# Optimization experiments

Hardware: AMD Instinct MI355X
Metric: run time of the kernel (lower is better)

## Reference

```python
import jax, jax.numpy as jnp
import numpy as np

B, N, D = 4, 256, 256
NEG = -1e9


def setup_inputs() -> dict:
    key = jax.random.key(0)
    k = jax.random.split(key, 5)
    scale1 = 1.0 / np.sqrt(4 * D)
    scale2 = 1.0 / np.sqrt(D)
    return {
        "shared": jax.random.normal(k[0], (B, N, D), dtype=jnp.float32),
        "W1": jax.random.uniform(k[1], (4 * D, D), jnp.float32, -scale1, scale1),
        "b1": jax.random.uniform(k[2], (D,), jnp.float32, -scale1, scale1),
        "W2": jax.random.uniform(k[3], (D, 1), jnp.float32, -scale2, scale2),
        "b2": jax.random.uniform(k[4], (1,), jnp.float32, -scale2, scale2),
    }


def reference(shared, W1, b1, W2, b2):
    # Linear on concat([src, tgt, |src-tgt|, src*tgt]) == sum of per-block matmuls.
    Wa, Wb, Wc, Wd = W1[:D], W1[D:2 * D], W1[2 * D:3 * D], W1[3 * D:]
    src_t = jnp.einsum('bid,dh->bih', shared, Wa)        # [B,N,D]
    tgt_t = jnp.einsum('bjd,dh->bjh', shared, Wb)        # [B,N,D]
    diff = jnp.abs(shared[:, :, None, :] - shared[:, None, :, :])  # [B,N,N,D]
    prod = shared[:, :, None, :] * shared[:, None, :, :]           # [B,N,N,D]
    h = (src_t[:, :, None, :] + tgt_t[:, None, :, :]
         + jnp.einsum('bijd,dh->bijh', diff, Wc)
         + jnp.einsum('bijd,dh->bijh', prod, Wd) + b1)   # [B,N,N,D]
    h = jax.nn.silu(h)
    scores = jnp.einsum('bijh,h->bij', h, W2[:, 0]) + b2[0]  # [B,N,N]
    eye = jnp.eye(N, dtype=bool)[None]
    scores = jnp.where(eye, NEG, scores)
    return jax.nn.softmax(scores, axis=-1)
```

## Files before the change

### kernel.cpp

```cpp
#include <hip/hip_runtime.h>

#define BB 4
#define NN 256
#define DD 256
#define HH 256
#define NEGV -1.0e9f

typedef _Float16 half8 __attribute__((ext_vector_type(8)));
typedef __fp16   fp16x2 __attribute__((ext_vector_type(2)));
typedef float floatx4 __attribute__((ext_vector_type(4)));

__global__ __launch_bounds__(1024) void prep(const float* __restrict__ X,
                                             const float* __restrict__ W1,
                                             float* __restrict__ S,
                                             float* __restrict__ T,
                                             _Float16* __restrict__ Wst) {
  const int g = blockIdx.x;
  const int t = threadIdx.x;

  __shared__ float xr[4][256];
  __shared__ float part[2][4][4][256];

  if (t < 256) {
    const float wcv = W1[(size_t)(2 * DD + g) * HH + t];
    const float wdv = W1[(size_t)(3 * DD + g) * HH + t];
    const int ks = g >> 4;
    const int dd = g & 15;
    const int q  = dd >> 2;
    const int e  = (dd & 3) * 2;
    const int hgrp = t >> 4;
    const int ccw  = t & 15;
    _Float16* p = Wst + ((size_t)((ks * 16 + hgrp) * 4 + q) * 16 + ccw) * 8 + e;
    p[0] = (_Float16)wcv;
    p[1] = (_Float16)wdv;
  }

  const int row0 = g * 4;
  xr[t >> 8][t & 255] = X[(size_t)row0 * DD + t];
  __syncthreads();

  const int w    = t >> 6;
  const int lane = t & 63;
  const int r    = w >> 2;
  const int kq   = w & 3;
  const int h0   = lane * 4;
  const float* __restrict__ xrow = xr[r];
  const int dbase = kq * 64;

  float sa0 = 0.f, sa1 = 0.f, sa2 = 0.f, sa3 = 0.f;
  float sb0 = 0.f, sb1 = 0.f, sb2 = 0.f, sb3 = 0.f;
#pragma unroll 4
  for (int dd = 0; dd < 64; ++dd) {
    const int d = dbase + dd;
    const float4 wa = *(const float4*)&W1[(size_t)d * HH + h0];
    const float4 wb = *(const float4*)&W1[(size_t)(DD + d) * HH + h0];
    const float x = xrow[d];
    sa0 = fmaf(x, wa.x, sa0); sa1 = fmaf(x, wa.y, sa1);
    sa2 = fmaf(x, wa.z, sa2); sa3 = fmaf(x, wa.w, sa3);
    sb0 = fmaf(x, wb.x, sb0); sb1 = fmaf(x, wb.y, sb1);
    sb2 = fmaf(x, wb.z, sb2); sb3 = fmaf(x, wb.w, sb3);
  }
  *(float4*)&part[0][r][kq][h0] = make_float4(sa0, sa1, sa2, sa3);
  *(float4*)&part[1][r][kq][h0] = make_float4(sb0, sb1, sb2, sb3);
  __syncthreads();

  const int rr = t >> 8, hh = t & 255;
  S[(size_t)(row0 + rr) * HH + hh] =
      (part[0][rr][0][hh] + part[0][rr][1][hh]) +
      (part[0][rr][2][hh] + part[0][rr][3][hh]);
  T[(size_t)(row0 + rr) * HH + hh] =
      (part[1][rr][0][hh] + part[1][rr][1][hh]) +
      (part[1][rr][2][hh] + part[1][rr][3][hh]);
}

__device__ __forceinline__ half8 make_afrag(const float4 xi, const float4 xj) {
  fp16x2 p0 = __builtin_amdgcn_cvt_pkrtz(__builtin_fabsf(xi.x - xj.x), xi.x * xj.x);
  fp16x2 p1 = __builtin_amdgcn_cvt_pkrtz(__builtin_fabsf(xi.y - xj.y), xi.y * xj.y);
  fp16x2 p2 = __builtin_amdgcn_cvt_pkrtz(__builtin_fabsf(xi.z - xj.z), xi.z * xj.z);
  fp16x2 p3 = __builtin_amdgcn_cvt_pkrtz(__builtin_fabsf(xi.w - xj.w), xi.w * xj.w);
  uint4 u;
  u.x = __builtin_bit_cast(unsigned int, p0);
  u.y = __builtin_bit_cast(unsigned int, p1);
  u.z = __builtin_bit_cast(unsigned int, p2);
  u.w = __builtin_bit_cast(unsigned int, p3);
  return __builtin_bit_cast(half8, u);
}

#define MFMA16(af, bf, acc) acc = __builtin_amdgcn_mfma_f32_16x16x32_f16(af, bf, acc, 0, 0, 0)

template <int CTRL>
__device__ __forceinline__ float dpp_add(float v) {
  const int s = __builtin_amdgcn_update_dpp(0, __builtin_bit_cast(int, v),
                                            CTRL, 0xF, 0xF, true);
  return v + __builtin_bit_cast(float, s);
}

__global__ __launch_bounds__(512, 4) void score_mfma(
    const float* __restrict__ X,  const float* __restrict__ b1,
    const float* __restrict__ W2, const float* __restrict__ b2,
    const float* __restrict__ S,  const float* __restrict__ T,
    const _Float16* __restrict__ Wst, float* __restrict__ Sc) {

  const int beta = blockIdx.x;
  const int b    = blockIdx.y;
  int i, qt;
  if (beta < 64)       { qt = 0; i = beta; }
  else if (beta < 192) { qt = 1; i = beta - 64; }
  else if (beta < 384) { qt = 2; i = beta - 192; }
  else                 { qt = 3; i = beta - 384; }
  const int bi    = b * NN + i;
  const int jbase = qt * 64;
  const int isUp  = qt > (i >> 6);

  const int t     = threadIdx.x;
  const int lane  = t & 63;
  const int hg    = t >> 6;
  const int q     = lane >> 4;
  const int cc    = lane & 15;

  __shared__ __align__(16) float    xi_s[DD];
  __shared__ __align__(16) _Float16 Af[32768];
  __shared__ float pre_s[HH];
  __shared__ float pre2_s[HH];
  __shared__ float w2_s[HH];
  __shared__ float sc_s[8][64];

  if (t < 256) {
    xi_s[t]  = X[(size_t)bi * DD + t];
    pre_s[t] = S[(size_t)bi * HH + t] + b1[t];
  } else {
    const int u = t - 256;
    pre2_s[u] = T[(size_t)bi * HH + u] + b1[u];
    w2_s[u]   = W2[u];
  }

  const float* __restrict__ Tb = T + (size_t)b * NN * HH;
  const float* __restrict__ Sb = S + (size_t)b * NN * HH;

  const int jloc = t & 63;
  const int jg   = jloc >> 4;
  const int ccw  = jloc & 15;
  const float* __restrict__ xjrow = X + (size_t)(b * NN + jbase + jloc) * DD;

  const char* __restrict__ bsrc = (const char*)Wst + hg * 2048 + (size_t)lane * 16;

  half8 Bf0[4], Bf1[4];
#pragma unroll
  for (int u = 0; u < 4; ++u) {
    Bf0[u] = *(const half8*)(bsrc + (size_t)u * 16384);
    Bf1[u] = *(const half8*)(bsrc + (size_t)u * 16384 + 1024);
  }

  __syncthreads();

  {
    const int sgrp = t >> 6;
#pragma unroll
    for (int idx = 0; idx < 8; ++idx) {
      const int ksqg = sgrp * 8 + idx;
      const int d0   = ksqg * 4;
      const int kg   = ksqg >> 2;
      const int qw   = ksqg & 3;
      const float4 xi4 = *(const float4*)&xi_s[d0];
      const float4 xj4 = *(const float4*)(xjrow + d0);
      *(half8*)&Af[kg * 2048 + (jg * 4 + qw) * 128 + ccw * 8] = make_afrag(xi4, xj4);
    }
  }
  __syncthreads();

  floatx4 acc0[4], acc1[4];
#pragma unroll
  for (int u = 0; u < 4; ++u) { acc0[u] = (floatx4)0.f; acc1[u] = (floatx4)0.f; }

  const _Float16* ap0 = &Af[lane * 8];
  half8 An0 = *(const half8*)(ap0);
  half8 An1 = *(const half8*)(ap0 + 512);
  half8 An2 = *(const half8*)(ap0 + 1024);
  half8 An3 = *(const half8*)(ap0 + 1536);

#pragma unroll
  for (int kg = 0; kg < 16; ++kg) {
    const int s = kg & 3;
    const half8 Bc0 = Bf0[s], Bc1 = Bf1[s];
    const half8 Ac0 = An0, Ac1 = An1, Ac2 = An2, Ac3 = An3;
    if (kg < 12) {
      const char* bk = bsrc + (size_t)(kg + 4) * 16384;
      Bf0[s] = *(const half8*)(bk);
      Bf1[s] = *(const half8*)(bk + 1024);
    }
    if (kg < 15) {
      const _Float16* ap = &Af[(kg + 1) * 2048 + lane * 8];
      An0 = *(const half8*)(ap);
      An1 = *(const half8*)(ap + 512);
      An2 = *(const half8*)(ap + 1024);
      An3 = *(const half8*)(ap + 1536);
    }
    MFMA16(Ac0, Bc0, acc0[0]); MFMA16(Ac0, Bc1, acc1[0]);
    MFMA16(Ac1, Bc0, acc0[1]); MFMA16(Ac1, Bc1, acc1[1]);
    MFMA16(Ac2, Bc0, acc0[2]); MFMA16(Ac2, Bc1, acc1[2]);
    MFMA16(Ac3, Bc0, acc0[3]); MFMA16(Ac3, Bc1, acc1[3]);
  }

  const int h0   = hg * 32 + cc;
  const int h1   = h0 + 16;
  const int jrow = jbase + q * 4;

#define EPILOGUE(VROW, PRE) {                                                   \
    float tv0[16], tv1[16];                                                     \
    _Pragma("unroll")                                                           \
    for (int u = 0; u < 16; ++u) {                                              \
      const size_t j = (size_t)(jrow + (u >> 2) * 16 + (u & 3)) * HH;           \
      tv0[u] = VROW[j + h0];                                                    \
      tv1[u] = VROW[j + h1];                                                    \
    }                                                                           \
    const float w20 = w2_s[h0], pv0 = PRE[h0];                                  \
    const float w21 = w2_s[h1], pv1 = PRE[h1];                                  \
    float p[16];                                                                \
    _Pragma("unroll")                                                           \
    for (int u = 0; u < 16; ++u) {                                              \
      const float hv0 = acc0[u >> 2][u & 3] + pv0 + tv0[u];                     \
      const float sv0 = hv0 * __builtin_amdgcn_rcpf(1.f + __expf(-hv0));        \
      p[u] = sv0 * w20;                                                         \
      const float hv1 = acc1[u >> 2][u & 3] + pv1 + tv1[u];                     \
      const float sv1 = hv1 * __builtin_amdgcn_rcpf(1.f + __expf(-hv1));        \
      p[u] = fmaf(sv1, w21, p[u]);                                              \
    }                                                                           \
    _Pragma("unroll")                                                           \
    for (int u = 0; u < 16; ++u) {                                              \
      float v = p[u];                                                           \
      v = dpp_add<0xB1>(v);                       \
      v = dpp_add<0x4E>(v);                       \
      v = dpp_add<0x141>(v);              \
      v = dpp_add<0x140>(v);                   \
      if (cc == 0) sc_s[hg][(u >> 2) * 16 + q * 4 + (u & 3)] = v;               \
    } }

  EPILOGUE(Tb, pre_s)
  __syncthreads();

  if (t < 64) {
    float s = sc_s[0][t] + sc_s[1][t] + sc_s[2][t] + sc_s[3][t]
            + sc_s[4][t] + sc_s[5][t] + sc_s[6][t] + sc_s[7][t] + b2[0];
    const int jg2 = jbase + t;
    if (jg2 == i) s = NEGV;
    Sc[(size_t)bi * NN + jg2] = s;
  }

  if (isUp) {
    __syncthreads();
    EPILOGUE(Sb, pre2_s)
    __syncthreads();
    if (t < 64) {
      const float s = sc_s[0][t] + sc_s[1][t] + sc_s[2][t] + sc_s[3][t]
                    + sc_s[4][t] + sc_s[5][t] + sc_s[6][t] + sc_s[7][t] + b2[0];
      Sc[(size_t)(b * NN + jbase + t) * NN + i] = s;
    }
  }
#undef EPILOGUE
}

__global__ __launch_bounds__(256) void softmax_kernel(const float* __restrict__ Sc,
                                                      float* __restrict__ out) {
  const int w    = threadIdx.x >> 6;
  const int lane = threadIdx.x & 63;
  const int bi   = blockIdx.x * 4 + w;
  const float4 v = *(const float4*)&Sc[(size_t)bi * NN + lane * 4];
  float m = fmaxf(fmaxf(v.x, v.y), fmaxf(v.z, v.w));
  m = fmaxf(m, __shfl_xor(m, 1));  m = fmaxf(m, __shfl_xor(m, 2));
  m = fmaxf(m, __shfl_xor(m, 4));  m = fmaxf(m, __shfl_xor(m, 8));
  m = fmaxf(m, __shfl_xor(m, 16)); m = fmaxf(m, __shfl_xor(m, 32));
  const float e0 = __expf(v.x - m), e1 = __expf(v.y - m);
  const float e2 = __expf(v.z - m), e3 = __expf(v.w - m);
  float sum = (e0 + e1) + (e2 + e3);
  sum += __shfl_xor(sum, 1);  sum += __shfl_xor(sum, 2);
  sum += __shfl_xor(sum, 4);  sum += __shfl_xor(sum, 8);
  sum += __shfl_xor(sum, 16); sum += __shfl_xor(sum, 32);
  const float r = 1.f / sum;
  float4 o; o.x = e0 * r; o.y = e1 * r; o.z = e2 * r; o.w = e3 * r;
  *(float4*)&out[(size_t)bi * NN + lane * 4] = o;
}

extern "C" void kernel_launch(void* const* d_in, const int* in_sizes, int n_in,
                              void* d_out, int out_size, void* d_ws, size_t ws_size,
                              hipStream_t stream) {
  const float* X  = (const float*)d_in[0];
  const float* W1 = (const float*)d_in[1];
  const float* b1 = (const float*)d_in[2];
  const float* W2 = (const float*)d_in[3];
  const float* b2 = (const float*)d_in[4];
  float* out = (float*)d_out;

  float*     Sws = (float*)d_ws;
  float*     Tws = Sws + (size_t)BB * NN * HH;
  _Float16*  Wst = (_Float16*)(Tws + (size_t)BB * NN * HH);
  float*     Scw = (float*)(Wst + (size_t)16 * HH * 32);

  prep<<<256, 1024, 0, stream>>>(X, W1, Sws, Tws, Wst);
  score_mfma<<<dim3(640, BB), 512, 0, stream>>>(X, b1, W2, b2, Sws, Tws, Wst, Scw);
  softmax_kernel<<<BB * NN / 4, 256, 0, stream>>>(Scw, out);
}
```

Measured before the change: 155.0 us.

## Retile pair-score MFMA warps to 2x4 j-by-h split with fewer LDS A loads

Changes the per-warp tile from all 64 j rows by 32 h columns to 32 j rows by 64 h columns. Each warp now reads two A fragments per k-step from LDS instead of four, and four B fragments from global (double-buffered) instead of two. The epilogue accumulates over h in registers before the cross-lane DPP reduction, so the shared partial-sum buffer and final reduction shrink to four partials per j. In exchange each warp issues more global weight loads and the prefetch depth drops from four stages to two.

```diff
diff --git a/kernel.cpp b/kernel.cpp
--- a/kernel.cpp
+++ b/kernel.cpp
@@ -114,7 +114,9 @@
 
   const int t     = threadIdx.x;
   const int lane  = t & 63;
-  const int hg    = t >> 6;
+  const int w     = t >> 6;
+  const int jh    = w >> 2;
+  const int hq    = w & 3;
   const int q     = lane >> 4;
   const int cc    = lane & 15;
 
@@ -123,7 +125,7 @@
   __shared__ float pre_s[HH];
   __shared__ float pre2_s[HH];
   __shared__ float w2_s[HH];
-  __shared__ float sc_s[8][64];
+  __shared__ float sc_s[8][32];
 
   if (t < 256) {
     xi_s[t]  = X[(size_t)bi * DD + t];
@@ -142,22 +144,21 @@
   const int ccw  = jloc & 15;
   const float* __restrict__ xjrow = X + (size_t)(b * NN + jbase + jloc) * DD;
 
-  const char* __restrict__ bsrc = (const char*)Wst + hg * 2048 + (size_t)lane * 16;
-
-  half8 Bf0[4], Bf1[4];
-#pragma unroll
-  for (int u = 0; u < 4; ++u) {
-    Bf0[u] = *(const half8*)(bsrc + (size_t)u * 16384);
-    Bf1[u] = *(const half8*)(bsrc + (size_t)u * 16384 + 1024);
-  }
+  const char* __restrict__ bsrc = (const char*)Wst + hq * 4096 + (size_t)lane * 16;
+
+  half8 Bf[2][4];
+#pragma unroll
+  for (int d = 0; d < 2; ++d)
+#pragma unroll
+    for (int m = 0; m < 4; ++m)
+      Bf[d][m] = *(const half8*)(bsrc + (size_t)d * 16384 + m * 1024);
 
   __syncthreads();
 
   {
-    const int sgrp = t >> 6;
 #pragma unroll
     for (int idx = 0; idx < 8; ++idx) {
-      const int ksqg = sgrp * 8 + idx;
+      const int ksqg = w * 8 + idx;
       const int d0   = ksqg * 4;
       const int kg   = ksqg >> 2;
       const int qw   = ksqg & 3;
@@ -172,75 +173,82 @@
 #pragma unroll
   for (int u = 0; u < 4; ++u) { acc0[u] = (floatx4)0.f; acc1[u] = (floatx4)0.f; }
 
-  const _Float16* ap0 = &Af[lane * 8];
+  const _Float16* ap0 = &Af[jh * 1024 + lane * 8];
   half8 An0 = *(const half8*)(ap0);
   half8 An1 = *(const half8*)(ap0 + 512);
-  half8 An2 = *(const half8*)(ap0 + 1024);
-  half8 An3 = *(const half8*)(ap0 + 1536);
 
 #pragma unroll
   for (int kg = 0; kg < 16; ++kg) {
-    const int s = kg & 3;
-    const half8 Bc0 = Bf0[s], Bc1 = Bf1[s];
-    const half8 Ac0 = An0, Ac1 = An1, Ac2 = An2, Ac3 = An3;
-    if (kg < 12) {
-      const char* bk = bsrc + (size_t)(kg + 4) * 16384;
-      Bf0[s] = *(const half8*)(bk);
-      Bf1[s] = *(const half8*)(bk + 1024);
+    const int s = kg & 1;
+    const half8 Bc0 = Bf[s][0], Bc1 = Bf[s][1];
+    const half8 Bc2 = Bf[s][2], Bc3 = Bf[s][3];
+    const half8 Ac0 = An0, Ac1 = An1;
+    if (kg < 14) {
+      const char* bk = bsrc + (size_t)(kg + 2) * 16384;
+#pragma unroll
+      for (int m = 0; m < 4; ++m)
+        Bf[s][m] = *(const half8*)(bk + m * 1024);
     }
     if (kg < 15) {
-      const _Float16* ap = &Af[(kg + 1) * 2048 + lane * 8];
+      const _Float16* ap = &Af[(kg + 1) * 2048 + jh * 1024 + lane * 8];
       An0 = *(const half8*)(ap);
       An1 = *(const half8*)(ap + 512);
-      An2 = *(const half8*)(ap + 1024);
-      An3 = *(const half8*)(ap + 1536);
     }
-    MFMA16(Ac0, Bc0, acc0[0]); MFMA16(Ac0, Bc1, acc1[0]);
-    MFMA16(Ac1, Bc0, acc0[1]); MFMA16(Ac1, Bc1, acc1[1]);
-    MFMA16(Ac2, Bc0, acc0[2]); MFMA16(Ac2, Bc1, acc1[2]);
-    MFMA16(Ac3, Bc0, acc0[3]); MFMA16(Ac3, Bc1, acc1[3]);
-  }
-
-  const int h0   = hg * 32 + cc;
-  const int h1   = h0 + 16;
-  const int jrow = jbase + q * 4;
+    MFMA16(Ac0, Bc0, acc0[0]); MFMA16(Ac0, Bc1, acc0[1]);
+    MFMA16(Ac0, Bc2, acc0[2]); MFMA16(Ac0, Bc3, acc0[3]);
+    MFMA16(Ac1, Bc0, acc1[0]); MFMA16(Ac1, Bc1, acc1[1]);
+    MFMA16(Ac1, Bc2, acc1[2]); MFMA16(Ac1, Bc3, acc1[3]);
+  }
+
+  const int hbase = hq * 64 + cc;
+  const int j0    = jbase + jh * 32 + q * 4;
 
 #define EPILOGUE(VROW, PRE) {                                                   \
     float tv0[16], tv1[16];                                                     \
     _Pragma("unroll")                                                           \
     for (int u = 0; u < 16; ++u) {                                              \
-      const size_t j = (size_t)(jrow + (u >> 2) * 16 + (u & 3)) * HH;           \
-      tv0[u] = VROW[j + h0];                                                    \
-      tv1[u] = VROW[j + h1];                                                    \
+      const size_t jrow = (size_t)(j0 + (u & 3)) * HH + hbase + (u >> 2) * 16;  \
+      tv0[u] = VROW[jrow];                                                      \
+      tv1[u] = VROW[jrow + (size_t)16 * HH];                                    \
     }                                                                           \
-    const float w20 = w2_s[h0], pv0 = PRE[h0];                                  \
-    const float w21 = w2_s[h1], pv1 = PRE[h1];                                  \
-    float p[16];                                                                \
+    float w2v[4], pv[4];                                                        \
+    _Pragma("unroll")                                                           \
+    for (int m = 0; m < 4; ++m) {                                               \
+      w2v[m] = w2_s[hbase + m * 16];                                            \
+      pv[m]  = PRE[hbase + m * 16];                                             \
+    }                                                                           \
+    float p0[4], p1[4];                                                         \
+    _Pragma("unroll")                                                           \
+    for (int r = 0; r < 4; ++r) { p0[r] = 0.f; p1[r] = 0.f; }                   \
     _Pragma("unroll")                                                           \
     for (int u = 0; u < 16; ++u) {                                              \
-      const float hv0 = acc0[u >> 2][u & 3] + pv0 + tv0[u];                     \
+      const int m = u >> 2, r = u & 3;                                          \
+      const float hv0 = acc0[m][r] + pv[m] + tv0[u];                            \
       const float sv0 = hv0 * __builtin_amdgcn_rcpf(1.f + __expf(-hv0));        \
-      p[u] = sv0 * w20;                                                         \
-      const float hv1 = acc1[u >> 2][u & 3] + pv1 + tv1[u];                     \
+      p0[r] = fmaf(sv0, w2v[m], p0[r]);                                         \
+      const float hv1 = acc1[m][r] + pv[m] + tv1[u];                            \
       const float sv1 = hv1 * __builtin_amdgcn_rcpf(1.f + __expf(-hv1));        \
-      p[u] = fmaf(sv1, w21, p[u]);                                              \
+      p1[r] = fmaf(sv1, w2v[m], p1[r]);                                         \
     }                                                                           \
     _Pragma("unroll")                                                           \
-    for (int u = 0; u < 16; ++u) {                                              \
-      float v = p[u];                                                           \
-      v = dpp_add<0xB1>(v);                       \
-      v = dpp_add<0x4E>(v);                       \
-      v = dpp_add<0x141>(v);              \
-      v = dpp_add<0x140>(v);                   \
-      if (cc == 0) sc_s[hg][(u >> 2) * 16 + q * 4 + (u & 3)] = v;               \
+    for (int r = 0; r < 4; ++r) {                                               \
+      float v = p0[r];                                                          \
+      v = dpp_add<0xB1>(v);  v = dpp_add<0x4E>(v);                              \
+      v = dpp_add<0x141>(v); v = dpp_add<0x140>(v);                             \
+      if (cc == 0) sc_s[w][q * 4 + r] = v;                                      \
+      float v2 = p1[r];                                                         \
+      v2 = dpp_add<0xB1>(v2);  v2 = dpp_add<0x4E>(v2);                          \
+      v2 = dpp_add<0x141>(v2); v2 = dpp_add<0x140>(v2);                         \
+      if (cc == 0) sc_s[w][16 + q * 4 + r] = v2;                                \
     } }
 
   EPILOGUE(Tb, pre_s)
   __syncthreads();
 
   if (t < 64) {
-    float s = sc_s[0][t] + sc_s[1][t] + sc_s[2][t] + sc_s[3][t]
-            + sc_s[4][t] + sc_s[5][t] + sc_s[6][t] + sc_s[7][t] + b2[0];
+    const int jh2 = t >> 5, jl = t & 31;
+    float s = (sc_s[jh2 * 4 + 0][jl] + sc_s[jh2 * 4 + 1][jl]) +
+              (sc_s[jh2 * 4 + 2][jl] + sc_s[jh2 * 4 + 3][jl]) + b2[0];
     const int jg2 = jbase + t;
     if (jg2 == i) s = NEGV;
     Sc[(size_t)bi * NN + jg2] = s;
@@ -251,8 +259,9 @@
     EPILOGUE(Sb, pre2_s)
     __syncthreads();
     if (t < 64) {
-      const float s = sc_s[0][t] + sc_s[1][t] + sc_s[2][t] + sc_s[3][t]
-                    + sc_s[4][t] + sc_s[5][t] + sc_s[6][t] + sc_s[7][t] + b2[0];
+      const int jh2 = t >> 5, jl = t & 31;
+      const float s = (sc_s[jh2 * 4 + 0][jl] + sc_s[jh2 * 4 + 1][jl]) +
+                      (sc_s[jh2 * 4 + 2][jl] + sc_s[jh2 * 4 + 3][jl]) + b2[0];
       Sc[(size_t)(b * NN + jbase + t) * NN + i] = s;
     }
   }
```

New measurement: 157.6 us. Within noise of the previous version (+1.7%).
